# Kernel optimization log

Hardware: AMD Instinct MI355X
Metric: run time of the kernel (lower is better)

## Reference

```python
import jax, jax.numpy as jnp
import numpy as np

C = 64
EPS = 1e-5


def conv3x3(x, w, groups=1):
    # x: NCHW, w: OIHW, stride 1, padding 1, dilation 1 (matches the torch code)
    return jax.lax.conv_general_dilated(
        x, w, window_strides=(1, 1), padding=((1, 1), (1, 1)),
        dimension_numbers=('NCHW', 'OIHW', 'NCHW'), feature_group_count=groups)


def shared_conv(x, w_shared):
    # SharedConv: one (1,1,3,3) filter applied to every channel == depthwise conv
    # with the weight broadcast across channels (replaces the per-channel loop).
    w = jnp.broadcast_to(w_shared, (C, 1, 3, 3))
    return conv3x3(x, w, groups=C)


def sdc(x, w_sh, w_d, b_d):
    s = shared_conv(x, w_sh)
    d = conv3x3(s + x, w_d) + b_d[None, :, None, None]
    return d + x


def batch_norm(x, gamma, beta):
    # training-mode BatchNorm2d: batch statistics over (N, H, W), biased var
    mean = jnp.mean(x, axis=(0, 2, 3), keepdims=True)
    var = jnp.var(x, axis=(0, 2, 3), keepdims=True)
    xn = (x - mean) * jax.lax.rsqrt(var + EPS)
    return gamma[None, :, None, None] * xn + beta[None, :, None, None]


def setup_inputs() -> dict:
    key = jax.random.key(0)
    ks = jax.random.split(key, 7)
    fan_sh = 1 * 3 * 3
    fan_d = C * 3 * 3
    inp = {
        'x': jax.random.normal(ks[0], (4, C, 224, 224), dtype=jnp.float32),
        'w_sh1': jax.random.normal(ks[1], (1, 1, 3, 3), dtype=jnp.float32) / np.sqrt(fan_sh),
        'w_d1': jax.random.normal(ks[2], (C, C, 3, 3), dtype=jnp.float32) / np.sqrt(fan_d),
        'b_d1': jnp.zeros((C,), dtype=jnp.float32),
        'w_sh2': jax.random.normal(ks[3], (1, 1, 3, 3), dtype=jnp.float32) / np.sqrt(fan_sh),
        'w_d2': jax.random.normal(ks[4], (C, C, 3, 3), dtype=jnp.float32) / np.sqrt(fan_d),
        'b_d2': jnp.zeros((C,), dtype=jnp.float32),
        'gamma1': jnp.ones((C,), dtype=jnp.float32),
        'beta1': jnp.zeros((C,), dtype=jnp.float32),
        'gamma2': jnp.ones((C,), dtype=jnp.float32),
        'beta2': jnp.zeros((C,), dtype=jnp.float32),
    }
    return inp


def reference(x, w_sh1, w_d1, b_d1, w_sh2, w_d2, b_d2, gamma1, beta1, gamma2, beta2):
    o1 = sdc(x, w_sh1, w_d1, b_d1)
    o1 = jax.nn.relu(batch_norm(o1, gamma1, beta1))
    o2 = sdc(o1, w_sh2, w_d2, b_d2)
    o2 = jax.nn.relu(batch_norm(o2, gamma2, beta2))
    return o2 + x
```

## Files before the change

### kernel.cpp

```cpp
#include <hip/hip_runtime.h>

#define N_ 4
#define C_ 64
#define H_ 224
#define W_ 224
#define HW_ (H_ * W_)
#define CHW_ (C_ * HW_)
#define TOT_ (N_ * CHW_)

typedef __bf16 bf8 __attribute__((ext_vector_type(8)));
typedef float  f4v __attribute__((ext_vector_type(4)));
typedef unsigned short u16;

__device__ __forceinline__ float relu_(float v) { return fmaxf(v, 0.f); }
__device__ __forceinline__ u16 f2bf(float f) {
    unsigned u = __builtin_bit_cast(unsigned, f);
    return (u16)((u + 0x7FFFu + ((u >> 16) & 1u)) >> 16);
}
__device__ __forceinline__ float bf2f(u16 h) {
    unsigned u = ((unsigned)h) << 16;
    return __builtin_bit_cast(float, u);
}
__device__ __forceinline__ float bflo(unsigned u) {
    return __builtin_bit_cast(float, u << 16);
}
__device__ __forceinline__ float bfhi(unsigned u) {
    return __builtin_bit_cast(float, u & 0xFFFF0000u);
}

__device__ __forceinline__ void gl_lds16(const void* g, void* l) {
    __builtin_amdgcn_global_load_lds(
        (const __attribute__((address_space(1))) void*)g,
        (__attribute__((address_space(3))) void*)l, 16, 0, 0);
}

__global__ __launch_bounds__(256) void prep_w(
    const float* __restrict__ wd1, const float* __restrict__ wd2,
    u16* __restrict__ wpre)
{
    int i = blockIdx.x * 256 + threadIdx.x;
    if (i >= 73728) return;
    int sel = i >= 36864;
    int r   = i - sel * 36864;
    int tap = r >> 12;
    int r2  = r & 4095;
    int o   = r2 >> 6, k = r2 & 63;
    const float* ws = sel ? wd2 : wd1;
    wpre[i] = f2bf(ws[o * 576 + k * 9 + tap]);
}

__global__ __launch_bounds__(256) void tpass1(
    const float* __restrict__ x, const float* __restrict__ wsh,
    u16* __restrict__ th)
{
    __shared__ unsigned TL[32][36];

    float wk[9];
#pragma unroll
    for (int k = 0; k < 9; ++k) wk[k] = wsh[k];
    const float wc1 = wk[4] + 1.f;

    const int orig = blockIdx.x;
    const int swz  = (orig & 7) * 784 + (orig >> 3);
    const int n    = swz / 1568;
    const int rem  = swz - n * 1568;
    const int row  = rem / 7;
    const int strip = rem - row * 7;

    const int tid = threadIdx.x;
    const int qd = tid & 7;
    const int c2 = tid >> 3;
    const int w0 = strip * 32 + qd * 4;
    const bool ym = row > 0, yp = row < H_ - 1;
    const bool xm = w0 > 0, xp = w0 + 4 < W_;

    float tq[2][4];
#pragma unroll
    for (int s = 0; s < 2; ++s) {
        const int ch = c2 * 2 + s;
        const float* bp = x + (size_t)n * CHW_ + (size_t)ch * HW_ + row * W_ + w0;

        float m0[4] = {0,0,0,0}, m1[4], m2[4] = {0,0,0,0};
        float l0 = 0.f, r0 = 0.f, l1 = 0.f, r1 = 0.f, l2 = 0.f, r2 = 0.f;
        if (ym) {
            float4 v = *(const float4*)(bp - W_);
            m0[0] = v.x; m0[1] = v.y; m0[2] = v.z; m0[3] = v.w;
            if (xm) l0 = bp[-W_ - 1];
            if (xp) r0 = bp[-W_ + 4];
        }
        {
            float4 v = *(const float4*)bp;
            m1[0] = v.x; m1[1] = v.y; m1[2] = v.z; m1[3] = v.w;
            if (xm) l1 = bp[-1];
            if (xp) r1 = bp[4];
        }
        if (yp) {
            float4 v = *(const float4*)(bp + W_);
            m2[0] = v.x; m2[1] = v.y; m2[2] = v.z; m2[3] = v.w;
            if (xm) l2 = bp[W_ - 1];
            if (xp) r2 = bp[W_ + 4];
        }
#pragma unroll
        for (int j = 0; j < 4; ++j) {
            float a0 = (j == 0) ? l0 : m0[j - 1];
            float a2 = (j == 3) ? r0 : m0[j + 1];
            float b0 = (j == 0) ? l1 : m1[j - 1];
            float b2 = (j == 3) ? r1 : m1[j + 1];
            float c0 = (j == 0) ? l2 : m2[j - 1];
            float c2v = (j == 3) ? r2 : m2[j + 1];
            float t = wc1 * m1[j];
            t = fmaf(wk[0], a0,    t);
            t = fmaf(wk[1], m0[j], t);
            t = fmaf(wk[2], a2,    t);
            t = fmaf(wk[3], b0,    t);
            t = fmaf(wk[5], b2,    t);
            t = fmaf(wk[6], c0,    t);
            t = fmaf(wk[7], m2[j], t);
            t = fmaf(wk[8], c2v,   t);
            tq[s][j] = t;
        }
    }
#pragma unroll
    for (int j = 0; j < 4; ++j)
        TL[qd * 4 + j][c2] = (unsigned)f2bf(tq[0][j]) | ((unsigned)f2bf(tq[1][j]) << 16);
    __syncthreads();

    const int px = tid >> 3, s = tid & 7;
    uint4 v = *(const uint4*)&TL[px][s * 4];
    *(uint4*)(th + (size_t)(n * HW_ + row * W_ + strip * 32 + px) * 64 + s * 8) = v;
}

__global__ __launch_bounds__(256) void tpass2(
    const u16* __restrict__ inh, const float* __restrict__ wsh,
    const float* __restrict__ raw, const float* __restrict__ gamma,
    const float* __restrict__ beta, u16* __restrict__ th)
{
    __shared__ float SS[128];
    const int tid = threadIdx.x;
    if (tid < 64) {
        const float cnt = (float)(N_ * HW_);
        float mean = raw[tid] / cnt;
        float var  = raw[64 + tid] / cnt - mean * mean;
        float inv  = rsqrtf(var + 1e-5f);
        float scv  = gamma[tid] * inv;
        SS[tid]      = scv;
        SS[64 + tid] = fmaf(-scv, mean, beta[tid]);
    }
    __syncthreads();

    float wk[9];
#pragma unroll
    for (int k = 0; k < 9; ++k) wk[k] = wsh[k];
    const float wc1 = wk[4] + 1.f;

    const int f0 = blockIdx.x * 256 + tid;
    const int s = f0 & 7;
    const int c0 = s * 8;
    float sc[8], sh[8];
#pragma unroll
    for (int j = 0; j < 8; ++j) { sc[j] = SS[c0 + j]; sh[j] = SS[64 + c0 + j]; }

    const int gsz = gridDim.x * 256;
    const int up = -64 * W_, dn = 64 * W_;

    for (int f = f0; f < TOT_ / 8; f += gsz) {
        const int pp = f >> 3;
        const int pix = pp % HW_;
        const int gh = pix / W_, gw = pix - gh * W_;
        const bool ym = gh > 0, yp = gh < H_ - 1, xm = gw > 0, xp = gw < W_ - 1;
        const u16* b = inh + (size_t)pp * 64 + c0;

        float t[8] = { 0.f, 0.f, 0.f, 0.f, 0.f, 0.f, 0.f, 0.f };
        auto acc8 = [&](int off, float wgt) {
            uint4 v = *(const uint4*)(b + off);
            unsigned wd_[4] = { v.x, v.y, v.z, v.w };
#pragma unroll
            for (int j = 0; j < 4; ++j) {
                float lo = bflo(wd_[j]), hi = bfhi(wd_[j]);
                t[2 * j]     = fmaf(wgt, relu_(fmaf(sc[2 * j], lo, sh[2 * j])), t[2 * j]);
                t[2 * j + 1] = fmaf(wgt, relu_(fmaf(sc[2 * j + 1], hi, sh[2 * j + 1])), t[2 * j + 1]);
            }
        };
        acc8(0, wc1);
        if (ym && xm) acc8(up - 64, wk[0]);
        if (ym)       acc8(up,      wk[1]);
        if (ym && xp) acc8(up + 64, wk[2]);
        if (xm)       acc8(-64,     wk[3]);
        if (xp)       acc8(64,      wk[5]);
        if (yp && xm) acc8(dn - 64, wk[6]);
        if (yp)       acc8(dn,      wk[7]);
        if (yp && xp) acc8(dn + 64, wk[8]);

        uint4 pk;
        pk.x = (unsigned)f2bf(t[0]) | ((unsigned)f2bf(t[1]) << 16);
        pk.y = (unsigned)f2bf(t[2]) | ((unsigned)f2bf(t[3]) << 16);
        pk.z = (unsigned)f2bf(t[4]) | ((unsigned)f2bf(t[5]) << 16);
        pk.w = (unsigned)f2bf(t[6]) | ((unsigned)f2bf(t[7]) << 16);
        *(uint4*)(th + (size_t)pp * 64 + c0) = pk;
    }
}

template<int LAYER>
__global__ __launch_bounds__(256, 3) void conv_mfma(
    const u16* __restrict__ th, const u16* __restrict__ wpre,
    const float* __restrict__ bd,
    const float* __restrict__ rawin, const float* __restrict__ gamma,
    const float* __restrict__ beta,
    const float* __restrict__ resx, const u16* __restrict__ reso,
    const u16* __restrict__ zp,
    u16* __restrict__ dsth, float* __restrict__ dstf,
    float* __restrict__ raw)
{
    __shared__ __align__(16) char TlB[340 * 128];
    __shared__ float Sr[128];
    __shared__ float SS[128];

    const int tid = threadIdx.x;
    const int orig = blockIdx.x;
    const int swz  = (orig & 7) * 98 + (orig >> 3);
    const int wx   = swz % 7;
    const int t_   = swz / 7;
    const int n    = t_ / 28;
    const int hy   = t_ - n * 28;
    const int h0 = hy * 8, w0 = wx * 32;

    const int lane = tid & 63, wg = tid >> 6;
    const int l15 = lane & 15, lg = lane >> 4;
    const int o = wg * 16 + l15;

    if (LAYER == 2 && tid < 64) {
        const float cnt = (float)(N_ * HW_);
        float mean = rawin[tid] / cnt;
        float var  = rawin[64 + tid] / cnt - mean * mean;
        float inv  = rsqrtf(var + 1e-5f);
        float scv  = gamma[tid] * inv;
        SS[tid]      = scv;
        SS[64 + tid] = fmaf(-scv, mean, beta[tid]);
    }

    bf8 B[18];
#pragma unroll
    for (int tap = 0; tap < 9; ++tap)
#pragma unroll
        for (int cc = 0; cc < 2; ++cc)
            B[tap * 2 + cc] = *(const bf8*)(wpre + ((tap * 64 + o) * 64 + cc * 32 + lg * 8));

#pragma unroll
    for (int it = 0; it < 11; ++it) {
        const int f = it * 256 + tid;
        if (f < 2720) {
            const int pix = f >> 3, s = f & 7;
            const int hr = pix / 34, wc = pix - hr * 34;
            const int gh = h0 - 1 + hr, gw = w0 - 1 + wc;
            const u16* src = zp;
            if ((unsigned)gh < (unsigned)H_ && (unsigned)gw < (unsigned)W_)
                src = th + (size_t)(n * HW_ + gh * W_ + gw) * 64 +
                      ((s * 8) ^ ((pix & 7) << 3));
            gl_lds16(src, TlB + (size_t)(it * 256 + (tid & 192)) * 16);
        }
    }
    __syncthreads();

    f4v acc[16];
#pragma unroll
    for (int mf = 0; mf < 16; ++mf) acc[mf] = (f4v){0.f, 0.f, 0.f, 0.f};

#pragma unroll
    for (int mf = 0; mf < 16; ++mf) {
        const int h = mf >> 1, half = mf & 1;
#pragma unroll
        for (int tap = 0; tap < 9; ++tap) {
            const int dr = tap / 3, dc = tap - dr * 3;
            const int hp = (h + dr) * 34 + half * 16 + dc + l15;
#pragma unroll
            for (int cc = 0; cc < 2; ++cc) {
                const bf8 A = *(const bf8*)(TlB + hp * 128 +
                                            ((cc * 64 + lg * 16) ^ ((hp & 7) << 4)));
                acc[mf] = __builtin_amdgcn_mfma_f32_16x16x32_bf16(
                    A, B[tap * 2 + cc], acc[mf], 0, 0, 0);
            }
        }
    }

    const float bv = bd[o];
    float scO = 1.f, shO = 0.f;
    if (LAYER == 2) { scO = SS[o]; shO = SS[64 + o]; }
    float ps1 = 0.f, ps2 = 0.f;
#pragma unroll
    for (int mf = 0; mf < 16; ++mf) {
        const int h = h0 + (mf >> 1);
        const int w = w0 + (mf & 1) * 16 + lg * 4;
        const int ppix = n * HW_ + h * W_ + w;
        float vo[4];
        if (LAYER == 1) {
            const float4 rx = *(const float4*)(resx + (size_t)n * CHW_ + (size_t)o * HW_ + h * W_ + w);
            vo[0] = acc[mf][0] + bv + rx.x;
            vo[1] = acc[mf][1] + bv + rx.y;
            vo[2] = acc[mf][2] + bv + rx.z;
            vo[3] = acc[mf][3] + bv + rx.w;
#pragma unroll
            for (int r = 0; r < 4; ++r)
                dsth[(size_t)(ppix + r) * 64 + o] = f2bf(vo[r]);
        } else {
#pragma unroll
            for (int r = 0; r < 4; ++r) {
                float n1 = relu_(fmaf(scO, bf2f(reso[(size_t)(ppix + r) * 64 + o]), shO));
                vo[r] = acc[mf][r] + bv + n1;
            }
            float4 st = { vo[0], vo[1], vo[2], vo[3] };
            *(float4*)(dstf + (size_t)n * CHW_ + (size_t)o * HW_ + h * W_ + w) = st;
        }
        ps1 += (vo[0] + vo[1]) + (vo[2] + vo[3]);
        ps2 += fmaf(vo[0], vo[0], fmaf(vo[1], vo[1], fmaf(vo[2], vo[2], vo[3] * vo[3])));
    }
    ps1 += __shfl_xor(ps1, 16); ps1 += __shfl_xor(ps1, 32);
    ps2 += __shfl_xor(ps2, 16); ps2 += __shfl_xor(ps2, 32);
    if (lane < 16) { Sr[o] = ps1; Sr[64 + o] = ps2; }
    __syncthreads();
    if (tid < 128) atomicAdd(&raw[tid], Sr[tid]);
}

__global__ __launch_bounds__(256) void final_k(
    float4* io, const float* __restrict__ raw, const float* __restrict__ gamma,
    const float* __restrict__ beta, const float4* __restrict__ x)
{
    __shared__ float SS[128];
    if (threadIdx.x < 64) {
        const int c = threadIdx.x;
        const float cnt = (float)(N_ * HW_);
        float mean = raw[c] / cnt;
        float var  = raw[64 + c] / cnt - mean * mean;
        float inv  = rsqrtf(var + 1e-5f);
        float scv  = gamma[c] * inv;
        SS[c]      = scv;
        SS[64 + c] = fmaf(-scv, mean, beta[c]);
    }
    __syncthreads();

    const int nq = TOT_ / 4;
    for (int i = blockIdx.x * 256 + threadIdx.x; i < nq; i += gridDim.x * 256) {
        int c = (i / (HW_ / 4)) & 63;
        float sc = SS[c], sh = SS[64 + c];
        float4 v = io[i], xx = x[i];
        float4 rr;
        rr.x = relu_(fmaf(sc, v.x, sh)) + xx.x;
        rr.y = relu_(fmaf(sc, v.y, sh)) + xx.y;
        rr.z = relu_(fmaf(sc, v.z, sh)) + xx.z;
        rr.w = relu_(fmaf(sc, v.w, sh)) + xx.w;
        io[i] = rr;
    }
}

extern "C" void kernel_launch(void* const* d_in, const int* in_sizes, int n_in,
                              void* d_out, int out_size, void* d_ws, size_t ws_size,
                              hipStream_t stream)
{
    const float* x    = (const float*)d_in[0];
    const float* wsh1 = (const float*)d_in[1];
    const float* wd1  = (const float*)d_in[2];
    const float* bd1  = (const float*)d_in[3];
    const float* wsh2 = (const float*)d_in[4];
    const float* wd2  = (const float*)d_in[5];
    const float* bd2  = (const float*)d_in[6];
    const float* g1   = (const float*)d_in[7];
    const float* be1  = (const float*)d_in[8];
    const float* g2   = (const float*)d_in[9];
    const float* be2  = (const float*)d_in[10];

    float* out = (float*)d_out;
    u16* Th   = (u16*)d_ws;
    u16* O1h  = Th + TOT_;
    u16* Wpre = O1h + TOT_;
    float* raw1 = (float*)(Wpre + 73728);
    float* raw2 = raw1 + 128;
    u16*   zp   = (u16*)(raw2 + 128);

    hipMemsetAsync(raw1, 0, 256 * sizeof(float) + 128, stream);
    prep_w<<<288, 256, 0, stream>>>(wd1, wd2, Wpre);

    const int t1grid = N_ * H_ * 7;
    const int cgrid = 784;

    tpass1<<<t1grid, 256, 0, stream>>>(x, wsh1, Th);
    conv_mfma<1><<<cgrid, 256, 0, stream>>>(Th, Wpre, bd1,
                                            nullptr, nullptr, nullptr,
                                            x, nullptr, zp, O1h, nullptr, raw1);
    tpass2<<<2048, 256, 0, stream>>>(O1h, wsh2, raw1, g1, be1, Th);
    conv_mfma<2><<<cgrid, 256, 0, stream>>>(Th, Wpre + 36864, bd2,
                                            raw1, g1, be1,
                                            nullptr, O1h, zp, nullptr, out, raw2);
    final_k<<<2048, 256, 0, stream>>>((float4*)out, raw2, g2, be2, (const float4*)x);
}
```

Before: 168.4 us.

## Store layer-1 output as fp32 NCHW and unify shared-conv passes

Layer-1 conv now writes its output as fp32 NCHW into the output buffer with coalesced float4 stores, replacing the bf16 NHWC intermediate that was written with scattered 2-byte stores. The second shared-conv pass reuses the tpass1 kernel, templated to apply BN+ReLU on load, and layer-2 conv reads its residual in place from the same buffer. This removes the strided per-channel bf16 writes and reads and a workspace buffer. In exchange the intermediate traffic doubles in bytes, and reading and writing the output in place requires dropping __restrict__.

```diff
diff --git a/kernel.cpp b/kernel.cpp
--- a/kernel.cpp
+++ b/kernel.cpp
@@ -20,12 +20,6 @@
 __device__ __forceinline__ float bf2f(u16 h) {
     unsigned u = ((unsigned)h) << 16;
     return __builtin_bit_cast(float, u);
-}
-__device__ __forceinline__ float bflo(unsigned u) {
-    return __builtin_bit_cast(float, u << 16);
-}
-__device__ __forceinline__ float bfhi(unsigned u) {
-    return __builtin_bit_cast(float, u & 0xFFFF0000u);
 }
 
 __device__ __forceinline__ void gl_lds16(const void* g, void* l) {
@@ -49,11 +43,28 @@
     wpre[i] = f2bf(ws[o * 576 + k * 9 + tap]);
 }
 
-__global__ __launch_bounds__(256) void tpass1(
-    const float* __restrict__ x, const float* __restrict__ wsh,
-    u16* __restrict__ th)
+template<bool NORM>
+__global__ __launch_bounds__(256) void tpass(
+    const float* __restrict__ in, const float* __restrict__ wsh,
+    const float* __restrict__ raw, const float* __restrict__ gamma,
+    const float* __restrict__ beta, u16* __restrict__ th)
 {
     __shared__ unsigned TL[32][36];
+    __shared__ float SS[128];
+
+    const int tid = threadIdx.x;
+    if (NORM) {
+        if (tid < 64) {
+            const float cnt = (float)(N_ * HW_);
+            float mean = raw[tid] / cnt;
+            float var  = raw[64 + tid] / cnt - mean * mean;
+            float inv  = rsqrtf(var + 1e-5f);
+            float scv  = gamma[tid] * inv;
+            SS[tid]      = scv;
+            SS[64 + tid] = fmaf(-scv, mean, beta[tid]);
+        }
+        __syncthreads();
+    }
 
     float wk[9];
 #pragma unroll
@@ -67,7 +78,6 @@
     const int row  = rem / 7;
     const int strip = rem - row * 7;
 
-    const int tid = threadIdx.x;
     const int qd = tid & 7;
     const int c2 = tid >> 3;
     const int w0 = strip * 32 + qd * 4;
@@ -78,27 +88,30 @@
 #pragma unroll
     for (int s = 0; s < 2; ++s) {
         const int ch = c2 * 2 + s;
-        const float* bp = x + (size_t)n * CHW_ + (size_t)ch * HW_ + row * W_ + w0;
+        float sc = 1.f, sh = 0.f;
+        if (NORM) { sc = SS[ch]; sh = SS[64 + ch]; }
+        auto nrm = [&](float v) { return NORM ? relu_(fmaf(sc, v, sh)) : v; };
+        const float* bp = in + (size_t)n * CHW_ + (size_t)ch * HW_ + row * W_ + w0;
 
         float m0[4] = {0,0,0,0}, m1[4], m2[4] = {0,0,0,0};
         float l0 = 0.f, r0 = 0.f, l1 = 0.f, r1 = 0.f, l2 = 0.f, r2 = 0.f;
         if (ym) {
             float4 v = *(const float4*)(bp - W_);
-            m0[0] = v.x; m0[1] = v.y; m0[2] = v.z; m0[3] = v.w;
-            if (xm) l0 = bp[-W_ - 1];
-            if (xp) r0 = bp[-W_ + 4];
+            m0[0] = nrm(v.x); m0[1] = nrm(v.y); m0[2] = nrm(v.z); m0[3] = nrm(v.w);
+            if (xm) l0 = nrm(bp[-W_ - 1]);
+            if (xp) r0 = nrm(bp[-W_ + 4]);
         }
         {
             float4 v = *(const float4*)bp;
-            m1[0] = v.x; m1[1] = v.y; m1[2] = v.z; m1[3] = v.w;
-            if (xm) l1 = bp[-1];
-            if (xp) r1 = bp[4];
+            m1[0] = nrm(v.x); m1[1] = nrm(v.y); m1[2] = nrm(v.z); m1[3] = nrm(v.w);
+            if (xm) l1 = nrm(bp[-1]);
+            if (xp) r1 = nrm(bp[4]);
         }
         if (yp) {
             float4 v = *(const float4*)(bp + W_);
-            m2[0] = v.x; m2[1] = v.y; m2[2] = v.z; m2[3] = v.w;
-            if (xm) l2 = bp[W_ - 1];
-            if (xp) r2 = bp[W_ + 4];
+            m2[0] = nrm(v.x); m2[1] = nrm(v.y); m2[2] = nrm(v.z); m2[3] = nrm(v.w);
+            if (xm) l2 = nrm(bp[W_ - 1]);
+            if (xp) r2 = nrm(bp[W_ + 4]);
         }
 #pragma unroll
         for (int j = 0; j < 4; ++j) {
@@ -130,85 +143,15 @@
     *(uint4*)(th + (size_t)(n * HW_ + row * W_ + strip * 32 + px) * 64 + s * 8) = v;
 }
 
-__global__ __launch_bounds__(256) void tpass2(
-    const u16* __restrict__ inh, const float* __restrict__ wsh,
-    const float* __restrict__ raw, const float* __restrict__ gamma,
-    const float* __restrict__ beta, u16* __restrict__ th)
-{
-    __shared__ float SS[128];
-    const int tid = threadIdx.x;
-    if (tid < 64) {
-        const float cnt = (float)(N_ * HW_);
-        float mean = raw[tid] / cnt;
-        float var  = raw[64 + tid] / cnt - mean * mean;
-        float inv  = rsqrtf(var + 1e-5f);
-        float scv  = gamma[tid] * inv;
-        SS[tid]      = scv;
-        SS[64 + tid] = fmaf(-scv, mean, beta[tid]);
-    }
-    __syncthreads();
-
-    float wk[9];
-#pragma unroll
-    for (int k = 0; k < 9; ++k) wk[k] = wsh[k];
-    const float wc1 = wk[4] + 1.f;
-
-    const int f0 = blockIdx.x * 256 + tid;
-    const int s = f0 & 7;
-    const int c0 = s * 8;
-    float sc[8], sh[8];
-#pragma unroll
-    for (int j = 0; j < 8; ++j) { sc[j] = SS[c0 + j]; sh[j] = SS[64 + c0 + j]; }
-
-    const int gsz = gridDim.x * 256;
-    const int up = -64 * W_, dn = 64 * W_;
-
-    for (int f = f0; f < TOT_ / 8; f += gsz) {
-        const int pp = f >> 3;
-        const int pix = pp % HW_;
-        const int gh = pix / W_, gw = pix - gh * W_;
-        const bool ym = gh > 0, yp = gh < H_ - 1, xm = gw > 0, xp = gw < W_ - 1;
-        const u16* b = inh + (size_t)pp * 64 + c0;
-
-        float t[8] = { 0.f, 0.f, 0.f, 0.f, 0.f, 0.f, 0.f, 0.f };
-        auto acc8 = [&](int off, float wgt) {
-            uint4 v = *(const uint4*)(b + off);
-            unsigned wd_[4] = { v.x, v.y, v.z, v.w };
-#pragma unroll
-            for (int j = 0; j < 4; ++j) {
-                float lo = bflo(wd_[j]), hi = bfhi(wd_[j]);
-                t[2 * j]     = fmaf(wgt, relu_(fmaf(sc[2 * j], lo, sh[2 * j])), t[2 * j]);
-                t[2 * j + 1] = fmaf(wgt, relu_(fmaf(sc[2 * j + 1], hi, sh[2 * j + 1])), t[2 * j + 1]);
-            }
-        };
-        acc8(0, wc1);
-        if (ym && xm) acc8(up - 64, wk[0]);
-        if (ym)       acc8(up,      wk[1]);
-        if (ym && xp) acc8(up + 64, wk[2]);
-        if (xm)       acc8(-64,     wk[3]);
-        if (xp)       acc8(64,      wk[5]);
-        if (yp && xm) acc8(dn - 64, wk[6]);
-        if (yp)       acc8(dn,      wk[7]);
-        if (yp && xp) acc8(dn + 64, wk[8]);
-
-        uint4 pk;
-        pk.x = (unsigned)f2bf(t[0]) | ((unsigned)f2bf(t[1]) << 16);
-        pk.y = (unsigned)f2bf(t[2]) | ((unsigned)f2bf(t[3]) << 16);
-        pk.z = (unsigned)f2bf(t[4]) | ((unsigned)f2bf(t[5]) << 16);
-        pk.w = (unsigned)f2bf(t[6]) | ((unsigned)f2bf(t[7]) << 16);
-        *(uint4*)(th + (size_t)pp * 64 + c0) = pk;
-    }
-}
-
 template<int LAYER>
 __global__ __launch_bounds__(256, 3) void conv_mfma(
     const u16* __restrict__ th, const u16* __restrict__ wpre,
     const float* __restrict__ bd,
     const float* __restrict__ rawin, const float* __restrict__ gamma,
     const float* __restrict__ beta,
-    const float* __restrict__ resx, const u16* __restrict__ reso,
+    const float* resx,
     const u16* __restrict__ zp,
-    u16* __restrict__ dsth, float* __restrict__ dstf,
+    float* dstf,
     float* __restrict__ raw)
 {
     __shared__ __align__(16) char TlB[340 * 128];
@@ -290,28 +233,22 @@
     for (int mf = 0; mf < 16; ++mf) {
         const int h = h0 + (mf >> 1);
         const int w = w0 + (mf & 1) * 16 + lg * 4;
-        const int ppix = n * HW_ + h * W_ + w;
-        float vo[4];
-        if (LAYER == 1) {
-            const float4 rx = *(const float4*)(resx + (size_t)n * CHW_ + (size_t)o * HW_ + h * W_ + w);
-            vo[0] = acc[mf][0] + bv + rx.x;
-            vo[1] = acc[mf][1] + bv + rx.y;
-            vo[2] = acc[mf][2] + bv + rx.z;
-            vo[3] = acc[mf][3] + bv + rx.w;
-#pragma unroll
-            for (int r = 0; r < 4; ++r)
-                dsth[(size_t)(ppix + r) * 64 + o] = f2bf(vo[r]);
-        } else {
-#pragma unroll
-            for (int r = 0; r < 4; ++r) {
-                float n1 = relu_(fmaf(scO, bf2f(reso[(size_t)(ppix + r) * 64 + o]), shO));
-                vo[r] = acc[mf][r] + bv + n1;
-            }
-            float4 st = { vo[0], vo[1], vo[2], vo[3] };
-            *(float4*)(dstf + (size_t)n * CHW_ + (size_t)o * HW_ + h * W_ + w) = st;
-        }
-        ps1 += (vo[0] + vo[1]) + (vo[2] + vo[3]);
-        ps2 += fmaf(vo[0], vo[0], fmaf(vo[1], vo[1], fmaf(vo[2], vo[2], vo[3] * vo[3])));
+        const size_t cidx = (size_t)n * CHW_ + (size_t)o * HW_ + h * W_ + w;
+        float4 rx = *(const float4*)(resx + cidx);
+        if (LAYER == 2) {
+            rx.x = relu_(fmaf(scO, rx.x, shO));
+            rx.y = relu_(fmaf(scO, rx.y, shO));
+            rx.z = relu_(fmaf(scO, rx.z, shO));
+            rx.w = relu_(fmaf(scO, rx.w, shO));
+        }
+        float4 st;
+        st.x = acc[mf][0] + bv + rx.x;
+        st.y = acc[mf][1] + bv + rx.y;
+        st.z = acc[mf][2] + bv + rx.z;
+        st.w = acc[mf][3] + bv + rx.w;
+        *(float4*)(dstf + cidx) = st;
+        ps1 += (st.x + st.y) + (st.z + st.w);
+        ps2 += fmaf(st.x, st.x, fmaf(st.y, st.y, fmaf(st.z, st.z, st.w * st.w)));
     }
     ps1 += __shfl_xor(ps1, 16); ps1 += __shfl_xor(ps1, 32);
     ps2 += __shfl_xor(ps2, 16); ps2 += __shfl_xor(ps2, 32);
@@ -369,8 +306,7 @@
 
     float* out = (float*)d_out;
     u16* Th   = (u16*)d_ws;
-    u16* O1h  = Th + TOT_;
-    u16* Wpre = O1h + TOT_;
+    u16* Wpre = Th + TOT_;
     float* raw1 = (float*)(Wpre + 73728);
     float* raw2 = raw1 + 128;
     u16*   zp   = (u16*)(raw2 + 128);
@@ -378,16 +314,16 @@
     hipMemsetAsync(raw1, 0, 256 * sizeof(float) + 128, stream);
     prep_w<<<288, 256, 0, stream>>>(wd1, wd2, Wpre);
 
-    const int t1grid = N_ * H_ * 7;
+    const int tgrid = N_ * H_ * 7;
     const int cgrid = 784;
 
-    tpass1<<<t1grid, 256, 0, stream>>>(x, wsh1, Th);
+    tpass<false><<<tgrid, 256, 0, stream>>>(x, wsh1, nullptr, nullptr, nullptr, Th);
     conv_mfma<1><<<cgrid, 256, 0, stream>>>(Th, Wpre, bd1,
                                             nullptr, nullptr, nullptr,
-                                            x, nullptr, zp, O1h, nullptr, raw1);
-    tpass2<<<2048, 256, 0, stream>>>(O1h, wsh2, raw1, g1, be1, Th);
+                                            x, zp, out, raw1);
+    tpass<true><<<tgrid, 256, 0, stream>>>(out, wsh2, raw1, g1, be1, Th);
     conv_mfma<2><<<cgrid, 256, 0, stream>>>(Th, Wpre + 36864, bd2,
                                             raw1, g1, be1,
-                                            nullptr, O1h, zp, nullptr, out, raw2);
+                                            out, zp, out, raw2);
     final_k<<<2048, 256, 0, stream>>>((float4*)out, raw2, g2, be2, (const float4*)x);
 }
```

After: 182.4 us. 1.08x slower.

## Reorder conv MFMA loop to reuse LDS A-fragments across rows and split weights by channel half

Applied to the files above, without the earlier changes.

The implicit-GEMM conv loop now iterates over input rows and loads each row's six A fragments from LDS once, reusing them for up to three output rows (dr taps). Previously each output row reloaded all nine tap fragments. Weight fragments are now loaded per channel half (9 registers instead of 18) inside a non-unrolled cc loop. This cuts LDS read traffic and register pressure, at the cost of an extra global weight load pass and less unrolling.

```diff
diff --git a/kernel.cpp b/kernel.cpp
--- a/kernel.cpp
+++ b/kernel.cpp
@@ -238,13 +238,6 @@
         SS[64 + tid] = fmaf(-scv, mean, beta[tid]);
     }
 
-    bf8 B[18];
-#pragma unroll
-    for (int tap = 0; tap < 9; ++tap)
-#pragma unroll
-        for (int cc = 0; cc < 2; ++cc)
-            B[tap * 2 + cc] = *(const bf8*)(wpre + ((tap * 64 + o) * 64 + cc * 32 + lg * 8));
-
 #pragma unroll
     for (int it = 0; it < 11; ++it) {
         const int f = it * 256 + tid;
@@ -265,19 +258,35 @@
 #pragma unroll
     for (int mf = 0; mf < 16; ++mf) acc[mf] = (f4v){0.f, 0.f, 0.f, 0.f};
 
-#pragma unroll
-    for (int mf = 0; mf < 16; ++mf) {
-        const int h = mf >> 1, half = mf & 1;
-#pragma unroll
-        for (int tap = 0; tap < 9; ++tap) {
-            const int dr = tap / 3, dc = tap - dr * 3;
-            const int hp = (h + dr) * 34 + half * 16 + dc + l15;
-#pragma unroll
-            for (int cc = 0; cc < 2; ++cc) {
-                const bf8 A = *(const bf8*)(TlB + hp * 128 +
-                                            ((cc * 64 + lg * 16) ^ ((hp & 7) << 4)));
-                acc[mf] = __builtin_amdgcn_mfma_f32_16x16x32_bf16(
-                    A, B[tap * 2 + cc], acc[mf], 0, 0, 0);
+#pragma unroll 1
+    for (int cc = 0; cc < 2; ++cc) {
+        bf8 Bt[9];
+#pragma unroll
+        for (int tap = 0; tap < 9; ++tap)
+            Bt[tap] = *(const bf8*)(wpre + ((tap * 64 + o) * 64 + cc * 32 + lg * 8));
+
+#pragma unroll
+        for (int ri = 0; ri < 10; ++ri) {
+            bf8 Af[2][3];
+#pragma unroll
+            for (int half = 0; half < 2; ++half)
+#pragma unroll
+                for (int dc = 0; dc < 3; ++dc) {
+                    const int hp = ri * 34 + half * 16 + dc + l15;
+                    Af[half][dc] = *(const bf8*)(TlB + hp * 128 +
+                                   ((cc * 64 + lg * 16) ^ ((hp & 7) << 4)));
+                }
+#pragma unroll
+            for (int dr = 0; dr < 3; ++dr) {
+                const int h = ri - dr;
+                if (h >= 0 && h < 8) {
+#pragma unroll
+                    for (int half = 0; half < 2; ++half)
+#pragma unroll
+                        for (int dc = 0; dc < 3; ++dc)
+                            acc[h * 2 + half] = __builtin_amdgcn_mfma_f32_16x16x32_bf16(
+                                Af[half][dc], Bt[dr * 3 + dc], acc[h * 2 + half], 0, 0, 0);
+                }
             }
         }
     }
@@ -378,10 +387,10 @@
     hipMemsetAsync(raw1, 0, 256 * sizeof(float) + 128, stream);
     prep_w<<<288, 256, 0, stream>>>(wd1, wd2, Wpre);
 
-    const int t1grid = N_ * H_ * 7;
+    const int tgrid = N_ * H_ * 7;
     const int cgrid = 784;
 
-    tpass1<<<t1grid, 256, 0, stream>>>(x, wsh1, Th);
+    tpass1<<<tgrid, 256, 0, stream>>>(x, wsh1, Th);
     conv_mfma<1><<<cgrid, 256, 0, stream>>>(Th, Wpre, bd1,
                                             nullptr, nullptr, nullptr,
                                             x, nullptr, zp, O1h, nullptr, raw1);
```

After: 248.6 us. 47.6% more time.
